# Performance work log

Hardware: AMD Instinct MI355X
Metric: run time of the kernel (lower is better)

## Reference

```python
import jax, jax.numpy as jnp
import numpy as np

# ----- static config (mirrors SteerableNCA defaults) -----
B, H, W = 4, 128, 128
HID = 12
C = HID + 5          # state channels = 17 (3 vis + 13 hidden + 1 angle)
WIDTH = 128          # update_width
STEPS = 48           # lower bound of num_dev_steps, fixed for jit
ALIVE_IDX = 3
ALIVE_THR = 0.1
UPDATE_P = 0.5
PC = 3 * C           # perception channels: [state, grad_x_rot, grad_y_rot]

SOBEL_X = jnp.array([[-1., 0., 1.], [-2., 0., 2.], [-1., 0., 1.]], jnp.float32) / 8.0
SOBEL_Y = SOBEL_X.T


def _dwconv3(x, k3):
    """Depthwise 3x3 conv with same padding. x: [B,C,H,W], k3: [3,3]."""
    c = x.shape[1]
    kern = jnp.broadcast_to(k3.astype(x.dtype), (c, 1, 3, 3))
    return jax.lax.conv_general_dilated(x, kern, (1, 1), 'SAME', feature_group_count=c)


def _maxpool3(x):
    """3x3 max pool, same padding. x: [B,H,W]."""
    return jax.lax.reduce_window(x, -jnp.inf, jax.lax.max, (1, 3, 3), (1, 1, 1), 'SAME')


def _radial_seed():
    """init_radial_seeds(n_seeds=2, seed_radius=4, vis=3, hidden=C-4, angle=1)."""
    vis, hid = 3, C - 4
    x = np.zeros((C, H, W), np.float32)
    t = np.linspace(0.0, 2.0 * np.pi, 2, endpoint=False).astype(np.float32)
    xy = np.stack([4.0 * np.cos(t), 4.0 * np.sin(t)], 0).astype(np.int32) + H // 2
    x[vis:vis + hid, xy[1], xy[0]] = 1.0
    x[-1, xy[1], xy[0]] = t
    return x


def setup_inputs() -> dict:
    key = jax.random.key(0)
    k1, k2, k3 = jax.random.split(key, 3)
    init_state = jnp.tile(jnp.asarray(_radial_seed())[None], (B, 1, 1, 1))
    rand = jax.random.uniform(k3, (STEPS, B, 1, H, W), jnp.float32)
    W1 = jax.random.normal(k1, (WIDTH, PC), jnp.float32) * 0.05
    b1 = jnp.zeros((WIDTH,), jnp.float32)
    W2 = jax.random.normal(k2, (C, WIDTH), jnp.float32) * 0.01
    b2 = jnp.zeros((C,), jnp.float32)
    return {"init_state": init_state, "rand": rand, "W1": W1, "b1": b1, "W2": W2, "b2": b2}


def reference(init_state, rand, W1, b1, W2, b2):
    def step(state, rnd):
        # --- steerable perception: rotate sobel gradients by per-cell angle ---
        angle = state[:, -1:]                       # [B,1,H,W]
        gx = _dwconv3(state, SOBEL_X)               # [B,C,H,W]
        gy = _dwconv3(state, SOBEL_Y)
        ca, sa = jnp.cos(angle), jnp.sin(angle)
        px = ca * gx + sa * gy
        py = -sa * gx + ca * gy
        p = jnp.concatenate([state, px, py], axis=1)  # [B,3C,H,W]
        # --- 1x1-conv MLP (Conv2d k=1 == channel GEMM) ---
        h = jax.nn.relu(jnp.einsum('oc,bchw->bohw', W1, p) + b1[None, :, None, None])
        dx = jnp.einsum('oc,bchw->bohw', W2, h) + b2[None, :, None, None]
        # --- stochastic alive-masked residual update ---
        pre_alive = _maxpool3(state[:, ALIVE_IDX]) > ALIVE_THR       # [B,H,W]
        upd_mask = (rnd < UPDATE_P).astype(state.dtype)              # [B,1,H,W]
        new = state + dx * upd_mask
        post_alive = _maxpool3(new[:, ALIVE_IDX]) > ALIVE_THR
        alive = (pre_alive & post_alive)[:, None].astype(state.dtype)
        new = new * alive
        return new, new

    final, dev_path = jax.lax.scan(step, init_state, rand)
    return final[:, :4], dev_path
```

## Files before the change

### kernel.cpp

```cpp
#include <hip/hip_runtime.h>

typedef _Float16 half8 __attribute__((ext_vector_type(8)));
typedef _Float16 half4v __attribute__((ext_vector_type(4)));
typedef float f32x4v __attribute__((ext_vector_type(4)));

#define Bn 4
#define Hn 128
#define Wn 128
#define HW (Hn*Wn)
#define Cn 17
#define STEPSn 48
#define NPIX (Bn*HW)
#define TY 4
#define TX 16

#define W1IMG_OFF 0
#define W2IMG_OFF 18432
#define ULAST_OFF 32768
#define FLAGS_OFF (ULAST_OFF + 4456448)

__global__ __launch_bounds__(256) void nca_prep(
    const float* __restrict__ W1, const float* __restrict__ W2,
    _Float16* __restrict__ w1img, _Float16* __restrict__ w2img)
{
  int t = blockIdx.x * 256 + threadIdx.x;
  if (t < 128 * 72) {
    int r = t / 72, k = t - r * 72;
    w1img[t] = (k < 51) ? (_Float16)W1[r * 51 + k] : (_Float16)0.f;
  } else {
    int u = t - 128 * 72;
    if (u < 32 * 128) {
      int r = u >> 7, k = u & 127;
      w2img[u] = (r < 17) ? (_Float16)W2[r * 128 + k] : (_Float16)0.f;
    }
  }
}

template<int MODE>
__global__ __launch_bounds__(256, 2) void nca_step(
    const float* __restrict__ prevU,
    const float* __restrict__ prev2,
    const float* __restrict__ rplane,
    const _Float16* __restrict__ w1img, const float* __restrict__ b1,
    const _Float16* __restrict__ w2img, const float* __restrict__ b2,
    float* __restrict__ outU, float* __restrict__ outM,
    const unsigned* __restrict__ flagsPrev, unsigned* __restrict__ flagsCur)
{
  __shared__ float Mt[Cn][6][24];
  __shared__ float pm[8][24], pu[8][24];
  __shared__ float alv[6][18];
  __shared__ _Float16 pscr[4][16][72];
  __shared__ _Float16 hscr[4][16][136];

  const int tid = threadIdx.x;
  const int w = tid >> 6, lane = tid & 63, l15 = lane & 15, g = lane >> 4;
  const int bx = blockIdx.x;
  const int b = bx >> 8;
  const int tIdx = bx & 255;
  const int ty = tIdx >> 3, tx = tIdx & 7;
  const int y0 = ty * TY, x0 = tx * TX;

  const float* ub = prevU + (size_t)b * Cn * HW;

  if (MODE) {
    int pred = 0;
    if (tid < 9) {
      int dy = tid / 3 - 1, dx = tid - (tid / 3) * 3 - 1;
      int nty = ty + dy, ntx = tx + dx;
      if ((unsigned)nty < 32u && (unsigned)ntx < 8u)
        pred = (int)flagsPrev[(b << 8) + nty * 8 + ntx];
    }
    int anyAct = __syncthreads_or(pred);
    if (!anyAct) {
      const f32x4v z = {0.f, 0.f, 0.f, 0.f};
      for (int task = tid; task < 68; task += 256) {
        int ch = task >> 2, r = task & 3;
        size_t base = (size_t)b * Cn * HW + ch * HW + (y0 + r) * Wn + x0;
        f32x4v* pU = (f32x4v*)(outU + base);
        f32x4v* pM = (f32x4v*)(outM + base);
        pU[0] = z; pU[1] = z; pU[2] = z; pU[3] = z;
        pM[0] = z; pM[1] = z; pM[2] = z; pM[3] = z;
      }
      if (tid == 0) flagsCur[bx] = 0u;
      return;
    }
  }

  half8 a1r[8][2]; f32x4v b1r[8];
#pragma unroll
  for (int m = 0; m < 8; ++m) {
#pragma unroll
    for (int kc = 0; kc < 2; ++kc)
      a1r[m][kc] = *(const half8*)(w1img + (m * 16 + l15) * 72 + kc * 32 + g * 8);
    b1r[m] = *(const f32x4v*)(b1 + m * 16 + g * 4);
  }
  half8 a2r[2][4];
#pragma unroll
  for (int m = 0; m < 2; ++m)
#pragma unroll
    for (int kc = 0; kc < 4; ++kc)
      a2r[m][kc] = *(const half8*)(w2img + (m * 16 + l15) * 128 + kc * 32 + g * 8);
  f32x4v b2v = *(const f32x4v*)(b2 + g * 4);
  float b2_16 = b2[16];

  for (int idx = lane; idx < 208; idx += 64) {
    int px = idx / 13, k = idx - px * 13 + 51;
    pscr[w][px][k] = (_Float16)0.f;
  }

  for (int task = tid; task < 408; task += 256) {
    int p = task >> 2, sl = task & 3;
    int ch = p / 6, r = p - ch * 6;
    int gy = y0 + r - 1;
    f32x4v v = {0.f, 0.f, 0.f, 0.f};
    if ((unsigned)gy < 128u)
      v = *(const f32x4v*)(ub + ch * HW + gy * Wn + x0 + sl * 4);
    *(f32x4v*)&Mt[ch][r][4 + sl * 4] = v;
  }
  for (int task = tid; task < 204; task += 256) {
    int p = task >> 1, side = task & 1;
    int ch = p / 6, r = p - ch * 6;
    int gy = y0 + r - 1, gx = side ? x0 + 16 : x0 - 1;
    float v = 0.f;
    if ((unsigned)gy < 128u && (unsigned)gx < 128u) v = ub[ch * HW + gy * Wn + gx];
    Mt[ch][r][side ? 20 : 3] = v;
  }
  if (MODE) {
    const float* u3 = ub + 3 * HW;
    const float* m3 = prev2 + ((size_t)b * Cn + 3) * HW;
    for (int task = tid; task < 64; task += 256) {
      int p = task >> 2, sl = task & 3;
      int py = p >> 1, pl = p & 1;
      int gy = y0 + py - 2;
      f32x4v v = {-1e30f, -1e30f, -1e30f, -1e30f};
      const float* src = pl ? u3 : m3;
      if ((unsigned)gy < 128u)
        v = *(const f32x4v*)(src + gy * Wn + x0 + sl * 4);
      float* dst = pl ? &pu[py][0] : &pm[py][0];
      *(f32x4v*)(dst + 4 + sl * 4) = v;
    }
    for (int task = tid; task < 64; task += 256) {
      int p = task >> 2, so = task & 3;
      int py = p >> 1, pl = p & 1;
      int gy = y0 + py - 2;
      int gx = (so < 2) ? (x0 + so - 2) : (x0 + so + 14);
      int ci = (so < 2) ? (so + 2) : (so + 18);
      float v = -1e30f;
      if ((unsigned)gy < 128u && (unsigned)gx < 128u) v = (pl ? u3 : m3)[gy * Wn + gx];
      (pl ? pu : pm)[py][ci] = v;
    }
  }
  __syncthreads();

  if (MODE) {
    if (tid < 108) {
      int my = tid / 18, mxi = tid - my * 18;
      float pre = -1e30f, post = -1e30f;
#pragma unroll
      for (int dy = 0; dy < 3; ++dy)
#pragma unroll
        for (int dxx = 0; dxx < 3; ++dxx) {
          pre  = fmaxf(pre,  pm[my + dy][mxi + 2 + dxx]);
          post = fmaxf(post, pu[my + dy][mxi + 2 + dxx]);
        }
      alv[my][mxi] = (pre > 0.1f && post > 0.1f) ? 1.f : 0.f;
    }
    __syncthreads();
    float* ob2 = outM + (size_t)b * Cn * HW;
    for (int task = tid; task < 1836; task += 256) {
      int ch = task / 108, cell = task - ch * 108;
      int my = cell / 18, mxi = cell - my * 18;
      float v = Mt[ch][my][mxi + 3] * alv[my][mxi];
      Mt[ch][my][mxi + 3] = v;
      if (my >= 1 && my <= 4 && mxi >= 1 && mxi <= 16)
        ob2[ch * HW + (y0 + my - 1) * Wn + (x0 + mxi - 1)] = v;
    }
    __syncthreads();
  }

  {
    const int my = w + 1, mtx = l15 + 4;
    float ang = Mt[16][my][mtx];
    float ca = cosf(ang), sa = sinf(ang);
#pragma unroll
    for (int j = 0; j < 5; ++j) {
      int c = g + 4 * j;
      if (c >= Cn) break;
      float n00 = Mt[c][my-1][mtx-1], n01 = Mt[c][my-1][mtx], n02 = Mt[c][my-1][mtx+1];
      float n10 = Mt[c][my  ][mtx-1], n11 = Mt[c][my  ][mtx], n12 = Mt[c][my  ][mtx+1];
      float n20 = Mt[c][my+1][mtx-1], n21 = Mt[c][my+1][mtx], n22 = Mt[c][my+1][mtx+1];
      float sx = (n02 - n00 + 2.f * (n12 - n10) + n22 - n20) * 0.125f;
      float sy = (n20 - n00 + 2.f * (n21 - n01) + n22 - n02) * 0.125f;
      pscr[w][l15][c]      = (_Float16)n11;
      pscr[w][l15][17 + c] = (_Float16)(ca * sx + sa * sy);
      pscr[w][l15][34 + c] = (_Float16)(ca * sy - sa * sx);
    }
  }
  asm volatile("s_waitcnt lgkmcnt(0)" ::: "memory");
  __builtin_amdgcn_sched_barrier(0);

  {
    half8 bf0 = *(const half8*)(&pscr[w][l15][g * 8]);
    half8 bf1 = *(const half8*)(&pscr[w][l15][32 + g * 8]);
#pragma unroll
    for (int m = 0; m < 8; ++m) {
      f32x4v acc = (f32x4v){0.f, 0.f, 0.f, 0.f};
      acc = __builtin_amdgcn_mfma_f32_16x16x32_f16(a1r[m][0], bf0, acc, 0, 0, 0);
      acc = __builtin_amdgcn_mfma_f32_16x16x32_f16(a1r[m][1], bf1, acc, 0, 0, 0);
      half4v hv;
#pragma unroll
      for (int i = 0; i < 4; ++i) hv[i] = (_Float16)fmaxf(acc[i] + b1r[m][i], 0.f);
      *(half4v*)(&hscr[w][l15][m * 16 + g * 4]) = hv;
    }
  }
  asm volatile("s_waitcnt lgkmcnt(0)" ::: "memory");
  __builtin_amdgcn_sched_barrier(0);

  f32x4v a2a = (f32x4v){0.f,0.f,0.f,0.f}, a2b = (f32x4v){0.f,0.f,0.f,0.f};
#pragma unroll
  for (int kc = 0; kc < 4; ++kc) {
    half8 bf = *(const half8*)(&hscr[w][l15][kc * 32 + g * 8]);
    a2a = __builtin_amdgcn_mfma_f32_16x16x32_f16(a2r[0][kc], bf, a2a, 0, 0, 0);
    a2b = __builtin_amdgcn_mfma_f32_16x16x32_f16(a2r[1][kc], bf, a2b, 0, 0, 0);
  }
  int nz = 0;
  {
    const int my = w + 1, mtx = l15 + 4;
    int gY = y0 + w, gX = x0 + l15;
    int ip = gY * Wn + gX;
    float upd = (rplane[(size_t)b * HW + ip] < 0.5f) ? 1.f : 0.f;
    float* ob = outU + (size_t)b * Cn * HW;
#pragma unroll
    for (int i = 0; i < 4; ++i) {
      float v = fmaf(a2a[i] + b2v[i], upd, Mt[g * 4 + i][my][mtx]);
      ob[(g * 4 + i) * HW + ip] = v;
      nz |= (v != 0.f);
    }
    if (g == 0) {
      float v = fmaf(a2b[0] + b2_16, upd, Mt[16][my][mtx]);
      ob[16 * HW + ip] = v;
      nz |= (v != 0.f);
    }
  }
  int anynz = __syncthreads_or(nz);
  if (tid == 0) flagsCur[bx] = anynz ? 1u : 0u;
}

__global__ __launch_bounds__(256) void nca_finalize(
    const float* __restrict__ U, const float* __restrict__ Mprev,
    float* __restrict__ Mout, float* __restrict__ final4)
{
  int t = blockIdx.x * 256 + threadIdx.x;
  int x = t & 127, y = (t >> 7) & 127, b = t >> 14;
  const float* u3 = U + ((size_t)b * Cn + 3) * HW;
  const float* m3 = Mprev + ((size_t)b * Cn + 3) * HW;
  float pre = -1e30f, post = -1e30f;
#pragma unroll
  for (int dy = -1; dy <= 1; ++dy) {
    int yy = y + dy; if ((unsigned)yy >= 128u) continue;
#pragma unroll
    for (int dxx = -1; dxx <= 1; ++dxx) {
      int xx = x + dxx; if ((unsigned)xx >= 128u) continue;
      pre = fmaxf(pre, m3[yy * Wn + xx]);
      post = fmaxf(post, u3[yy * Wn + xx]);
    }
  }
  float alive = (pre > 0.1f && post > 0.1f) ? 1.f : 0.f;
  int ip = y * Wn + x;
#pragma unroll
  for (int c = 0; c < Cn; ++c) {
    float v = U[((size_t)b * Cn + c) * HW + ip] * alive;
    Mout[((size_t)b * Cn + c) * HW + ip] = v;
    if (c < 4) final4[((size_t)b * 4 + c) * HW + ip] = v;
  }
}

extern "C" void kernel_launch(void* const* d_in, const int* in_sizes, int n_in,
                              void* d_out, int out_size, void* d_ws, size_t ws_size,
                              hipStream_t stream) {
  const float* init_state = (const float*)d_in[0];
  const float* rand_all   = (const float*)d_in[1];
  const float* W1 = (const float*)d_in[2];
  const float* b1 = (const float*)d_in[3];
  const float* W2 = (const float*)d_in[4];
  const float* b2 = (const float*)d_in[5];

  float* out = (float*)d_out;
  float* final4 = out;
  float* dev_path = out + (size_t)Bn * 4 * HW;
  char* ws = (char*)d_ws;
  _Float16* w1img = (_Float16*)(ws + W1IMG_OFF);
  _Float16* w2img = (_Float16*)(ws + W2IMG_OFF);
  float* Ulast = (float*)(ws + ULAST_OFF);
  unsigned* flags = (unsigned*)(ws + FLAGS_OFF);

  const size_t stateSz = (size_t)Bn * Cn * HW;
  auto slot = [&](int i) { return dev_path + (size_t)i * stateSz; };

  hipLaunchKernelGGL(nca_prep, dim3(52), dim3(256), 0, stream, W1, W2, w1img, w2img);

  hipLaunchKernelGGL((nca_step<0>), dim3(1024), dim3(256), 0, stream,
                     init_state, (const float*)nullptr, rand_all,
                     w1img, b1, w2img, b2, slot(1), (float*)nullptr,
                     (const unsigned*)nullptr, flags );
  for (int s = 1; s < STEPSn; ++s) {
    const float* prevU = slot(s);
    const float* prev2 = (s >= 2) ? slot(s - 2) : init_state;
    float* outU = (s < STEPSn - 1) ? slot(s + 1) : Ulast;
    hipLaunchKernelGGL((nca_step<1>), dim3(1024), dim3(256), 0, stream,
                       prevU, prev2, rand_all + (size_t)s * NPIX,
                       w1img, b1, w2img, b2, outU, slot(s - 1),
                       flags + ((s - 1) & 1) * 1024, flags + (s & 1) * 1024);
  }
  hipLaunchKernelGGL(nca_finalize, dim3(NPIX / 256), dim3(256), 0, stream,
                     Ulast, slot(STEPSn - 2), slot(STEPSn - 1), final4);
}
```

Baseline: 683.6 us.

## Issue all global tile loads before activity check and vectorize masked-state writeback

Global loads of the state tile, halo columns, alive-channel planes and the random plane are moved into registers at kernel start, before the neighbor-flag barrier, so their latency overlaps the skip check and weight loading. Values are then written into shared memory after the early-exit test. The masked-state writeback is restructured so each thread handles a whole row and emits float4 stores instead of scalar stores. This adds register pressure and issues loads even for tiles that will exit early.

```diff
diff --git a/kernel.cpp b/kernel.cpp
--- a/kernel.cpp
+++ b/kernel.cpp
@@ -62,14 +62,61 @@
 
   const float* ub = prevU + (size_t)b * Cn * HW;
 
+  f32x4v iv0 = {0.f, 0.f, 0.f, 0.f}, iv1 = {0.f, 0.f, 0.f, 0.f};
+  float hv = 0.f;
+  f32x4v pv = {-1e30f, -1e30f, -1e30f, -1e30f};
+  float phv = -1e30f;
+  int pred = 0;
+  {
+    int p = tid >> 2, sl = tid & 3;
+    int ch = p / 6, r = p - ch * 6;
+    int gy = y0 + r - 1;
+    if ((unsigned)gy < 128u)
+      iv0 = *(const f32x4v*)(ub + ch * HW + gy * Wn + x0 + sl * 4);
+  }
+  if (tid < 152) {
+    int task = tid + 256;
+    int p = task >> 2, sl = task & 3;
+    int ch = p / 6, r = p - ch * 6;
+    int gy = y0 + r - 1;
+    if ((unsigned)gy < 128u)
+      iv1 = *(const f32x4v*)(ub + ch * HW + gy * Wn + x0 + sl * 4);
+  }
+  if (tid < 204) {
+    int p = tid >> 1, side = tid & 1;
+    int ch = p / 6, r = p - ch * 6;
+    int gy = y0 + r - 1, gx = side ? x0 + 16 : x0 - 1;
+    if ((unsigned)gy < 128u && (unsigned)gx < 128u)
+      hv = ub[ch * HW + gy * Wn + gx];
+  }
   if (MODE) {
-    int pred = 0;
+    const float* u3 = ub + 3 * HW;
+    const float* m3 = prev2 + ((size_t)b * Cn + 3) * HW;
+    if (tid < 64) {
+      int p = tid >> 2, sl = tid & 3;
+      int py = p >> 1, pl = p & 1;
+      int gy = y0 + py - 2;
+      if ((unsigned)gy < 128u)
+        pv = *(const f32x4v*)((pl ? u3 : m3) + gy * Wn + x0 + sl * 4);
+    } else if (tid < 128) {
+      int t2 = tid - 64;
+      int p = t2 >> 2, so = t2 & 3;
+      int py = p >> 1, pl = p & 1;
+      int gy = y0 + py - 2;
+      int gx = (so < 2) ? (x0 + so - 2) : (x0 + so + 14);
+      if ((unsigned)gy < 128u && (unsigned)gx < 128u)
+        phv = (pl ? u3 : m3)[gy * Wn + gx];
+    }
     if (tid < 9) {
       int dy = tid / 3 - 1, dx = tid - (tid / 3) * 3 - 1;
       int nty = ty + dy, ntx = tx + dx;
       if ((unsigned)nty < 32u && (unsigned)ntx < 8u)
         pred = (int)flagsPrev[(b << 8) + nty * 8 + ntx];
     }
+  }
+  const float rv = rplane[(size_t)b * HW + (y0 + w) * Wn + x0 + l15];
+
+  if (MODE) {
     int anyAct = __syncthreads_or(pred);
     if (!anyAct) {
       const f32x4v z = {0.f, 0.f, 0.f, 0.f};
@@ -86,6 +133,36 @@
     }
   }
 
+  {
+    int p = tid >> 2, sl = tid & 3;
+    int ch = p / 6, r = p - ch * 6;
+    *(f32x4v*)&Mt[ch][r][4 + sl * 4] = iv0;
+  }
+  if (tid < 152) {
+    int task = tid + 256;
+    int p = task >> 2, sl = task & 3;
+    int ch = p / 6, r = p - ch * 6;
+    *(f32x4v*)&Mt[ch][r][4 + sl * 4] = iv1;
+  }
+  if (tid < 204) {
+    int p = tid >> 1, side = tid & 1;
+    int ch = p / 6, r = p - ch * 6;
+    Mt[ch][r][side ? 20 : 3] = hv;
+  }
+  if (MODE) {
+    if (tid < 64) {
+      int p = tid >> 2, sl = tid & 3;
+      int py = p >> 1, pl = p & 1;
+      *(f32x4v*)((pl ? &pu[py][0] : &pm[py][0]) + 4 + sl * 4) = pv;
+    } else if (tid < 128) {
+      int t2 = tid - 64;
+      int p = t2 >> 2, so = t2 & 3;
+      int py = p >> 1, pl = p & 1;
+      int ci = (so < 2) ? (so + 2) : (so + 18);
+      (pl ? pu : pm)[py][ci] = phv;
+    }
+  }
+
   half8 a1r[8][2]; f32x4v b1r[8];
 #pragma unroll
   for (int m = 0; m < 8; ++m) {
@@ -106,49 +183,6 @@
   for (int idx = lane; idx < 208; idx += 64) {
     int px = idx / 13, k = idx - px * 13 + 51;
     pscr[w][px][k] = (_Float16)0.f;
-  }
-
-  for (int task = tid; task < 408; task += 256) {
-    int p = task >> 2, sl = task & 3;
-    int ch = p / 6, r = p - ch * 6;
-    int gy = y0 + r - 1;
-    f32x4v v = {0.f, 0.f, 0.f, 0.f};
-    if ((unsigned)gy < 128u)
-      v = *(const f32x4v*)(ub + ch * HW + gy * Wn + x0 + sl * 4);
-    *(f32x4v*)&Mt[ch][r][4 + sl * 4] = v;
-  }
-  for (int task = tid; task < 204; task += 256) {
-    int p = task >> 1, side = task & 1;
-    int ch = p / 6, r = p - ch * 6;
-    int gy = y0 + r - 1, gx = side ? x0 + 16 : x0 - 1;
-    float v = 0.f;
-    if ((unsigned)gy < 128u && (unsigned)gx < 128u) v = ub[ch * HW + gy * Wn + gx];
-    Mt[ch][r][side ? 20 : 3] = v;
-  }
-  if (MODE) {
-    const float* u3 = ub + 3 * HW;
-    const float* m3 = prev2 + ((size_t)b * Cn + 3) * HW;
-    for (int task = tid; task < 64; task += 256) {
-      int p = task >> 2, sl = task & 3;
-      int py = p >> 1, pl = p & 1;
-      int gy = y0 + py - 2;
-      f32x4v v = {-1e30f, -1e30f, -1e30f, -1e30f};
-      const float* src = pl ? u3 : m3;
-      if ((unsigned)gy < 128u)
-        v = *(const f32x4v*)(src + gy * Wn + x0 + sl * 4);
-      float* dst = pl ? &pu[py][0] : &pm[py][0];
-      *(f32x4v*)(dst + 4 + sl * 4) = v;
-    }
-    for (int task = tid; task < 64; task += 256) {
-      int p = task >> 2, so = task & 3;
-      int py = p >> 1, pl = p & 1;
-      int gy = y0 + py - 2;
-      int gx = (so < 2) ? (x0 + so - 2) : (x0 + so + 14);
-      int ci = (so < 2) ? (so + 2) : (so + 18);
-      float v = -1e30f;
-      if ((unsigned)gy < 128u && (unsigned)gx < 128u) v = (pl ? u3 : m3)[gy * Wn + gx];
-      (pl ? pu : pm)[py][ci] = v;
-    }
   }
   __syncthreads();
 
@@ -166,14 +200,22 @@
       alv[my][mxi] = (pre > 0.1f && post > 0.1f) ? 1.f : 0.f;
     }
     __syncthreads();
-    float* ob2 = outM + (size_t)b * Cn * HW;
-    for (int task = tid; task < 1836; task += 256) {
-      int ch = task / 108, cell = task - ch * 108;
-      int my = cell / 18, mxi = cell - my * 18;
-      float v = Mt[ch][my][mxi + 3] * alv[my][mxi];
-      Mt[ch][my][mxi + 3] = v;
-      if (my >= 1 && my <= 4 && mxi >= 1 && mxi <= 16)
-        ob2[ch * HW + (y0 + my - 1) * Wn + (x0 + mxi - 1)] = v;
+    if (tid < 102) {
+      int ch = tid / 6, my = tid - ch * 6;
+      float vrow[18];
+#pragma unroll
+      for (int cI = 0; cI < 18; ++cI) {
+        float v = Mt[ch][my][cI + 3] * alv[my][cI];
+        Mt[ch][my][cI + 3] = v;
+        vrow[cI] = v;
+      }
+      if (my >= 1 && my <= 4) {
+        float* orow = outM + (size_t)b * Cn * HW + ch * HW + (y0 + my - 1) * Wn + x0;
+        *(f32x4v*)(orow +  0) = (f32x4v){vrow[ 1], vrow[ 2], vrow[ 3], vrow[ 4]};
+        *(f32x4v*)(orow +  4) = (f32x4v){vrow[ 5], vrow[ 6], vrow[ 7], vrow[ 8]};
+        *(f32x4v*)(orow +  8) = (f32x4v){vrow[ 9], vrow[10], vrow[11], vrow[12]};
+        *(f32x4v*)(orow + 12) = (f32x4v){vrow[13], vrow[14], vrow[15], vrow[16]};
+      }
     }
     __syncthreads();
   }
@@ -207,10 +249,10 @@
       f32x4v acc = (f32x4v){0.f, 0.f, 0.f, 0.f};
       acc = __builtin_amdgcn_mfma_f32_16x16x32_f16(a1r[m][0], bf0, acc, 0, 0, 0);
       acc = __builtin_amdgcn_mfma_f32_16x16x32_f16(a1r[m][1], bf1, acc, 0, 0, 0);
-      half4v hv;
-#pragma unroll
-      for (int i = 0; i < 4; ++i) hv[i] = (_Float16)fmaxf(acc[i] + b1r[m][i], 0.f);
-      *(half4v*)(&hscr[w][l15][m * 16 + g * 4]) = hv;
+      half4v hv2;
+#pragma unroll
+      for (int i = 0; i < 4; ++i) hv2[i] = (_Float16)fmaxf(acc[i] + b1r[m][i], 0.f);
+      *(half4v*)(&hscr[w][l15][m * 16 + g * 4]) = hv2;
     }
   }
   asm volatile("s_waitcnt lgkmcnt(0)" ::: "memory");
@@ -226,9 +268,8 @@
   int nz = 0;
   {
     const int my = w + 1, mtx = l15 + 4;
-    int gY = y0 + w, gX = x0 + l15;
-    int ip = gY * Wn + gX;
-    float upd = (rplane[(size_t)b * HW + ip] < 0.5f) ? 1.f : 0.f;
+    int ip = (y0 + w) * Wn + x0 + l15;
+    float upd = (rv < 0.5f) ? 1.f : 0.f;
     float* ob = outU + (size_t)b * Cn * HW;
 #pragma unroll
     for (int i = 0; i < 4; ++i) {
```

Result: faster. 579.8 us (-15.2%).
